# Performance work log

Measured on AMD Instinct MI355X. Metric: run time of the kernel, lower is better.

## Reference

```python
import jax, jax.numpy as jnp
import numpy as np

N = 500_000
D = 256
D_OUT = 256
B = 16_384


def setup_inputs() -> dict:
    key = jax.random.key(0)
    ks = jax.random.split(key, 10)
    x = jax.random.normal(ks[0], (N, D), dtype=jnp.float32)
    batch = jnp.sort(jax.random.randint(ks[1], (N,), 0, B))
    last_click_mask = jax.random.uniform(ks[2], (N,), dtype=jnp.float32)
    s = 1.0 / np.sqrt(D)
    W1 = jax.random.uniform(ks[3], (D, D), jnp.float32, -s, s)
    b1 = jax.random.uniform(ks[4], (D,), jnp.float32, -s, s)
    W2 = jax.random.uniform(ks[5], (D, D), jnp.float32, -s, s)
    b2 = jax.random.uniform(ks[6], (D,), jnp.float32, -s, s)
    w3 = jax.random.uniform(ks[7], (D, 1), jnp.float32, -s, s)
    s4 = 1.0 / np.sqrt(2 * D)
    W4 = jax.random.uniform(ks[8], (2 * D, D_OUT), jnp.float32, -s4, s4)
    b4 = jax.random.uniform(ks[9], (D_OUT,), jnp.float32, -s4, s4)
    return {
        "x": x,
        "batch": batch,
        "last_click_mask": last_click_mask,
        "num_segments": B,
        "W1": W1, "b1": b1, "W2": W2, "b2": b2,
        "w3": w3, "W4": W4, "b4": b4,
    }


def reference(x, batch, last_click_mask, num_segments, W1, b1, W2, b2, w3, W4, b4):
    # local_rep = global_add_pool(x * mask, batch)  -> [B, D]
    local_rep = jax.ops.segment_sum(x * last_click_mask[:, None], batch,
                                    num_segments=num_segments)
    local_rep_repeat = local_rep[batch]                       # [N, D] gather
    att = jax.nn.sigmoid(local_rep_repeat @ W1 + b1 + x @ W2 + b2) @ w3  # [N, 1]
    weighted_x = x * att                                      # [N, D]
    global_rep = jax.ops.segment_sum(weighted_x, batch,
                                     num_segments=num_segments)  # [B, D]
    rep = jnp.concatenate([local_rep, global_rep], axis=1)    # [B, 2D]
    return rep @ W4 + b4                                      # [B, D_OUT]
```

## Files before the change

### kernel.cpp

```cpp
#include <hip/hip_runtime.h>
#include <hip/hip_bf16.h>

#define NROWS 500000
#define DIM   256
#define BSEG  16384
#define LDSP  264

typedef __attribute__((ext_vector_type(8))) short short8;
typedef __attribute__((ext_vector_type(4))) float floatx4;


__device__ __forceinline__ unsigned short f2bf(float f) {
  unsigned u = __float_as_uint(f);
  unsigned r = u + 0x7fffu + ((u >> 16) & 1u);
  return (unsigned short)(r >> 16);
}
__device__ __forceinline__ float bf2f(short s) {
  return __uint_as_float(((unsigned)(unsigned short)s) << 16);
}
__device__ __forceinline__ float fast_sigmoid(float z) {
  return 1.0f / (1.0f + __expf(-z));
}

__global__ __launch_bounds__(1024) void k_zero(float* __restrict__ p, int n4) {
  int i = blockIdx.x * blockDim.x + threadIdx.x;
  if (i < n4) ((float4*)p)[i] = make_float4(0.f, 0.f, 0.f, 0.f);
}

__global__ __launch_bounds__(256) void k_convert_all(
    const float* __restrict__ W1, const float* __restrict__ W2,
    const float* __restrict__ W4, short* __restrict__ W1t,
    short* __restrict__ W2t, short* __restrict__ W4t)
{
  int blk = blockIdx.x;
  const float* W; short* out; int kt;
  if (blk < 8)       { W = W1; out = W1t; kt = blk; }
  else if (blk < 16) { W = W2; out = W2t; kt = blk - 8; }
  else               { W = W4; out = W4t; kt = blk - 16; }
  int n = threadIdx.x;
  short tmp[32];
#pragma unroll
  for (int kk = 0; kk < 32; ++kk)
    tmp[kk] = (short)f2bf(W[(size_t)(kt * 32 + kk) * DIM + n]);
  size_t base = ((size_t)kt * 256 + n) * 32;
#pragma unroll
  for (int kk = 0; kk < 32; kk += 4)
    *(short4*)&out[base + kk] = *(short4*)&tmp[kk];
}

__global__ __launch_bounds__(256) void k_seg_local(
    const float* __restrict__ x, const int* __restrict__ batch,
    const float* __restrict__ mask, float* __restrict__ local_rep,
    int rows_per_block)
{
  const int col = threadIdx.x;
  int r0 = blockIdx.x * rows_per_block;
  int r1 = min(NROWS, r0 + rows_per_block);
  if (r0 >= r1) return;
  float acc = 0.f;
  int cur = batch[r0];
  int r = r0;
  for (; r + 4 <= r1; r += 4) {
    float xv0 = x[(size_t)(r + 0) * DIM + col];
    float xv1 = x[(size_t)(r + 1) * DIM + col];
    float xv2 = x[(size_t)(r + 2) * DIM + col];
    float xv3 = x[(size_t)(r + 3) * DIM + col];
    int s0 = batch[r], s1 = batch[r + 1], s2 = batch[r + 2], s3 = batch[r + 3];
    float m0 = mask[r], m1 = mask[r + 1], m2 = mask[r + 2], m3 = mask[r + 3];
    if (s0 != cur) { atomicAdd(&local_rep[(size_t)cur * DIM + col], acc); acc = 0.f; cur = s0; }
    acc = fmaf(xv0, m0, acc);
    if (s1 != cur) { atomicAdd(&local_rep[(size_t)cur * DIM + col], acc); acc = 0.f; cur = s1; }
    acc = fmaf(xv1, m1, acc);
    if (s2 != cur) { atomicAdd(&local_rep[(size_t)cur * DIM + col], acc); acc = 0.f; cur = s2; }
    acc = fmaf(xv2, m2, acc);
    if (s3 != cur) { atomicAdd(&local_rep[(size_t)cur * DIM + col], acc); acc = 0.f; cur = s3; }
    acc = fmaf(xv3, m3, acc);
  }
  for (; r < r1; ++r) {
    int s = batch[r];
    float xv = x[(size_t)r * DIM + col];
    float mv = mask[r];
    if (s != cur) { atomicAdd(&local_rep[(size_t)cur * DIM + col], acc); acc = 0.f; cur = s; }
    acc = fmaf(xv, mv, acc);
  }
  atomicAdd(&local_rep[(size_t)cur * DIM + col], acc);
}

__device__ __forceinline__ void stage_tile(const float* __restrict__ A, int row0,
                                           int maxrow, short* xs, int tid)
{
#pragma unroll
  for (int it = 0; it < 16; ++it) {
    int linear = it * 256 + tid;
    int r = linear >> 6;
    int c4 = linear & 63;
    int row = min(row0 + r, maxrow);
    float4 v = *(const float4*)&A[(size_t)row * DIM + c4 * 4];
    short4 o;
    o.x = (short)f2bf(v.x); o.y = (short)f2bf(v.y);
    o.z = (short)f2bf(v.z); o.w = (short)f2bf(v.w);
    *(short4*)&xs[r * LDSP + c4 * 4] = o;
  }
}

__device__ __forceinline__ void mfma_pass(const short* xs, const short* __restrict__ Wt,
                                          floatx4 acc[4][4], int lane15, int quad, int n0)
{
  short8 bfr[2][4], afr[2][4];
#pragma unroll
  for (int jn = 0; jn < 4; ++jn)
    bfr[0][jn] = *(const short8*)&Wt[(size_t)(n0 + jn * 16 + lane15) * 32 + quad * 8];
#pragma unroll
  for (int i = 0; i < 4; ++i)
    afr[0][i] = *(const short8*)&xs[(i * 16 + lane15) * LDSP + quad * 8];

#pragma unroll
  for (int kt = 0; kt < 8; ++kt) {
    const int cur = kt & 1, nxt = cur ^ 1;
    if (kt < 7) {
      const int k2 = kt + 1;
#pragma unroll
      for (int jn = 0; jn < 4; ++jn)
        bfr[nxt][jn] = *(const short8*)&Wt[(size_t)k2 * 8192 + (n0 + jn * 16 + lane15) * 32 + quad * 8];
#pragma unroll
      for (int i = 0; i < 4; ++i)
        afr[nxt][i] = *(const short8*)&xs[(i * 16 + lane15) * LDSP + k2 * 32 + quad * 8];
    }
#pragma unroll
    for (int i = 0; i < 4; ++i)
#pragma unroll
      for (int jn = 0; jn < 4; ++jn)
        acc[i][jn] = __builtin_amdgcn_mfma_f32_16x16x32_bf16(afr[cur][i], bfr[cur][jn], acc[i][jn], 0, 0, 0);
  }
}

__global__ __launch_bounds__(256) void k_h1_mfma(
    const float* __restrict__ A, const short* __restrict__ Wt,
    const float* __restrict__ bias, short* __restrict__ H1bf)
{
  __shared__ short xs[64 * LDSP];
  const int tid = threadIdx.x;
  const int row0 = blockIdx.x * 64;
  stage_tile(A, row0, BSEG - 1, xs, tid);
  __syncthreads();
  const int lane = tid & 63, wave = tid >> 6;
  const int lane15 = lane & 15, quad = lane >> 4;
  const int n0 = wave * 64;
  floatx4 acc[4][4];
#pragma unroll
  for (int i = 0; i < 4; ++i)
#pragma unroll
    for (int j = 0; j < 4; ++j) acc[i][j] = (floatx4)0.f;
  mfma_pass(xs, Wt, acc, lane15, quad, n0);
#pragma unroll
  for (int i = 0; i < 4; ++i)
#pragma unroll
    for (int jn = 0; jn < 4; ++jn) {
      int col = n0 + jn * 16 + lane15;
      float bv = bias[col];
#pragma unroll
      for (int r = 0; r < 4; ++r) {
        int row = row0 + i * 16 + quad * 4 + r;
        H1bf[(size_t)row * DIM + col] = (short)f2bf(acc[i][jn][r] + bv);
      }
    }
}

__global__ __launch_bounds__(256) void k_fused_main(
    const float* __restrict__ x, const int* __restrict__ batch,
    const short* __restrict__ W2t, const float* __restrict__ b2,
    const float* __restrict__ w3, const short* __restrict__ H1bf,
    float* __restrict__ global_rep)
{
  __shared__ short xs[64 * LDSP];
  __shared__ int   seg_s[64];
  __shared__ float att_s[64];
  const int tid = threadIdx.x;
  const int row0 = blockIdx.x * 64;

  stage_tile(x, row0, NROWS - 1, xs, tid);
  if (tid < 64) {
    seg_s[tid] = batch[min(row0 + tid, NROWS - 1)];
    att_s[tid] = 0.f;
  }
  __syncthreads();

  const int lane = tid & 63, wave = tid >> 6;
  const int lane15 = lane & 15, quad = lane >> 4;
  const int n0 = wave * 64;
  floatx4 acc[4][4];
#pragma unroll
  for (int i = 0; i < 4; ++i)
#pragma unroll
    for (int j = 0; j < 4; ++j) acc[i][j] = (floatx4)0.f;
  mfma_pass(xs, W2t, acc, lane15, quad, n0);

  float b2v[4], w3v[4];
#pragma unroll
  for (int jn = 0; jn < 4; ++jn) {
    int col = n0 + jn * 16 + lane15;
    b2v[jn] = b2[col];
    w3v[jn] = w3[col];
  }
  float part[4][4];
#pragma unroll
  for (int i = 0; i < 4; ++i)
#pragma unroll
    for (int r = 0; r < 4; ++r) {
      int rl = i * 16 + quad * 4 + r;
      int seg = seg_s[rl];
      float p = 0.f;
#pragma unroll
      for (int jn = 0; jn < 4; ++jn) {
        int col = n0 + jn * 16 + lane15;
        float h = bf2f(H1bf[(size_t)seg * DIM + col]);
        float z = acc[i][jn][r] + h + b2v[jn];
        p = fmaf(fast_sigmoid(z), w3v[jn], p);
      }
      part[i][r] = p;
    }
#pragma unroll
  for (int off = 1; off < 16; off <<= 1)
#pragma unroll
    for (int i = 0; i < 4; ++i)
#pragma unroll
      for (int r = 0; r < 4; ++r)
        part[i][r] += __shfl_xor(part[i][r], off, 64);
  if (lane15 == 0) {
#pragma unroll
    for (int i = 0; i < 4; ++i)
#pragma unroll
      for (int r = 0; r < 4; ++r)
        atomicAdd(&att_s[i * 16 + quad * 4 + r], part[i][r]);
  }
  __syncthreads();

  const int col = tid;
  const int rmax = min(64, NROWS - row0);
  float acc2 = 0.f;
  int cur = seg_s[0];
  for (int r = 0; r < rmax; ++r) {
    int s = seg_s[r];
    float xv = bf2f(xs[r * LDSP + col]);
    float av = att_s[r];
    if (s != cur) {
      atomicAdd(&global_rep[(size_t)cur * DIM + col], acc2);
      acc2 = 0.f; cur = s;
    }
    acc2 = fmaf(xv, av, acc2);
  }
  atomicAdd(&global_rep[(size_t)cur * DIM + col], acc2);
}

__global__ __launch_bounds__(256) void k_out_mfma(
    const float* __restrict__ local_rep, const float* __restrict__ global_rep,
    const short* __restrict__ W4t, const float* __restrict__ b4,
    float* __restrict__ out)
{
  __shared__ short xs[64 * LDSP];
  const int tid = threadIdx.x;
  const int row0 = blockIdx.x * 64;
  const int lane = tid & 63, wave = tid >> 6;
  const int lane15 = lane & 15, quad = lane >> 4;
  const int n0 = wave * 64;
  floatx4 acc[4][4];
#pragma unroll
  for (int i = 0; i < 4; ++i)
#pragma unroll
    for (int j = 0; j < 4; ++j) acc[i][j] = (floatx4)0.f;

  stage_tile(local_rep, row0, BSEG - 1, xs, tid);
  __syncthreads();
  mfma_pass(xs, W4t, acc, lane15, quad, n0);
  __syncthreads();
  stage_tile(global_rep, row0, BSEG - 1, xs, tid);
  __syncthreads();
  mfma_pass(xs, W4t + (size_t)8 * 8192, acc, lane15, quad, n0);

#pragma unroll
  for (int i = 0; i < 4; ++i)
#pragma unroll
    for (int jn = 0; jn < 4; ++jn) {
      int col = n0 + jn * 16 + lane15;
      float bv = b4[col];
#pragma unroll
      for (int r = 0; r < 4; ++r) {
        int row = row0 + i * 16 + quad * 4 + r;
        out[(size_t)row * DIM + col] = acc[i][jn][r] + bv;
      }
    }
}

extern "C" void kernel_launch(void* const* d_in, const int* in_sizes, int n_in,
                              void* d_out, int out_size, void* d_ws, size_t ws_size,
                              hipStream_t stream) {
  (void)in_sizes; (void)n_in; (void)out_size; (void)ws_size;
  const float* x    = (const float*)d_in[0];
  const int*   batch= (const int*)d_in[1];
  const float* mask = (const float*)d_in[2];
  const float* W1 = (const float*)d_in[4];
  const float* b1 = (const float*)d_in[5];
  const float* W2 = (const float*)d_in[6];
  const float* b2 = (const float*)d_in[7];
  const float* w3 = (const float*)d_in[8];
  const float* W4 = (const float*)d_in[9];
  const float* b4 = (const float*)d_in[10];
  float* out = (float*)d_out;

  char* base = (char*)d_ws;
  float* local_rep  = (float*)(base);
  float* global_rep = (float*)(base + (size_t)16 * 1024 * 1024);
  short* H1bf       = (short*)(base + (size_t)32 * 1024 * 1024);
  short* W1t        = (short*)(base + (size_t)40 * 1024 * 1024);
  short* W2t        = (short*)(base + (size_t)40 * 1024 * 1024 + 128 * 1024);
  short* W4t        = (short*)(base + (size_t)40 * 1024 * 1024 + 256 * 1024);

  int n4 = 2 * BSEG * DIM / 4;
  hipLaunchKernelGGL(k_zero, dim3(n4 / 1024), dim3(1024), 0, stream, local_rep, n4);

  hipLaunchKernelGGL(k_convert_all, dim3(32), dim3(256), 0, stream,
                     W1, W2, W4, W1t, W2t, W4t);

  const int SEG_BLOCKS = 4096;
  int rpb = (NROWS + SEG_BLOCKS - 1) / SEG_BLOCKS;
  hipLaunchKernelGGL(k_seg_local, dim3(SEG_BLOCKS), dim3(256), 0, stream,
                     x, batch, mask, local_rep, rpb);

  hipLaunchKernelGGL(k_h1_mfma, dim3(BSEG / 64), dim3(256), 0, stream,
                     local_rep, W1t, b1, H1bf);

  hipLaunchKernelGGL(k_fused_main, dim3((NROWS + 63) / 64), dim3(256), 0, stream,
                     x, batch, W2t, b2, w3, H1bf, global_rep);

  hipLaunchKernelGGL(k_out_mfma, dim3(BSEG / 64), dim3(256), 0, stream,
                     local_rep, global_rep, W4t, b4, out);
}
```

Before: 1.023 ms.

## Pre-convert x to padded bf16 tiles and stream them into LDS directly

Replaces the strided segment-sum kernel with a tiled prep kernel. It stages each 64-row tile of x, converts it to bf16 and writes it out as a padded LDS image. It also computes the masked local segment sum from that tile. The main fused kernel then copies these bf16 tiles straight into LDS with global_load_lds instead of reloading fp32 x and converting it, which removes per-block conversion work and halves that kernel's input bytes. The MFMA inner loop also drops its register double-buffering, which reduces register pressure but may expose load latency. In exchange, the bf16 tile buffer is an extra write and read of roughly half the size of x, and local_rep is now summed from bf16-rounded x, which loses precision.

```diff
diff --git a/kernel.cpp b/kernel.cpp
--- a/kernel.cpp
+++ b/kernel.cpp
@@ -5,9 +5,16 @@
 #define DIM   256
 #define BSEG  16384
 #define LDSP  264
+#define NTILE 7813
+#define TILE_B (64 * LDSP * 2)
 
 typedef __attribute__((ext_vector_type(8))) short short8;
 typedef __attribute__((ext_vector_type(4))) float floatx4;
+
+#define GLD16(gsrc, ldst)                                                      \
+  __builtin_amdgcn_global_load_lds(                                            \
+      (const __attribute__((address_space(1))) unsigned int*)(gsrc),           \
+      (__attribute__((address_space(3))) unsigned int*)(ldst), 16, 0, 0)
 
 
 __device__ __forceinline__ unsigned short f2bf(float f) {
@@ -46,44 +53,6 @@
 #pragma unroll
   for (int kk = 0; kk < 32; kk += 4)
     *(short4*)&out[base + kk] = *(short4*)&tmp[kk];
-}
-
-__global__ __launch_bounds__(256) void k_seg_local(
-    const float* __restrict__ x, const int* __restrict__ batch,
-    const float* __restrict__ mask, float* __restrict__ local_rep,
-    int rows_per_block)
-{
-  const int col = threadIdx.x;
-  int r0 = blockIdx.x * rows_per_block;
-  int r1 = min(NROWS, r0 + rows_per_block);
-  if (r0 >= r1) return;
-  float acc = 0.f;
-  int cur = batch[r0];
-  int r = r0;
-  for (; r + 4 <= r1; r += 4) {
-    float xv0 = x[(size_t)(r + 0) * DIM + col];
-    float xv1 = x[(size_t)(r + 1) * DIM + col];
-    float xv2 = x[(size_t)(r + 2) * DIM + col];
-    float xv3 = x[(size_t)(r + 3) * DIM + col];
-    int s0 = batch[r], s1 = batch[r + 1], s2 = batch[r + 2], s3 = batch[r + 3];
-    float m0 = mask[r], m1 = mask[r + 1], m2 = mask[r + 2], m3 = mask[r + 3];
-    if (s0 != cur) { atomicAdd(&local_rep[(size_t)cur * DIM + col], acc); acc = 0.f; cur = s0; }
-    acc = fmaf(xv0, m0, acc);
-    if (s1 != cur) { atomicAdd(&local_rep[(size_t)cur * DIM + col], acc); acc = 0.f; cur = s1; }
-    acc = fmaf(xv1, m1, acc);
-    if (s2 != cur) { atomicAdd(&local_rep[(size_t)cur * DIM + col], acc); acc = 0.f; cur = s2; }
-    acc = fmaf(xv2, m2, acc);
-    if (s3 != cur) { atomicAdd(&local_rep[(size_t)cur * DIM + col], acc); acc = 0.f; cur = s3; }
-    acc = fmaf(xv3, m3, acc);
-  }
-  for (; r < r1; ++r) {
-    int s = batch[r];
-    float xv = x[(size_t)r * DIM + col];
-    float mv = mask[r];
-    if (s != cur) { atomicAdd(&local_rep[(size_t)cur * DIM + col], acc); acc = 0.f; cur = s; }
-    acc = fmaf(xv, mv, acc);
-  }
-  atomicAdd(&local_rep[(size_t)cur * DIM + col], acc);
 }
 
 __device__ __forceinline__ void stage_tile(const float* __restrict__ A, int row0,
@@ -103,34 +72,65 @@
   }
 }
 
+__global__ __launch_bounds__(256) void k_prep(
+    const float* __restrict__ x, const int* __restrict__ batch,
+    const float* __restrict__ mask, char* __restrict__ xbf16p,
+    float* __restrict__ local_rep)
+{
+  __shared__ __align__(16) short xs[64 * LDSP];
+  __shared__ int   seg_s[64];
+  __shared__ float mask_s[64];
+  const int tid = threadIdx.x;
+  const int tile = blockIdx.x;
+  const int row0 = tile * 64;
+
+  stage_tile(x, row0, NROWS - 1, xs, tid);
+  if (tid < 64) {
+    int row = min(row0 + tid, NROWS - 1);
+    seg_s[tid] = batch[row];
+    mask_s[tid] = mask[row];
+  }
+  __syncthreads();
+
+  float4* g4 = (float4*)(xbf16p + (size_t)tile * TILE_B);
+  const float4* l4 = (const float4*)xs;
+#pragma unroll
+  for (int j = 0; j < 8; ++j)
+    g4[j * 256 + tid] = l4[j * 256 + tid];
+  if (tid < 64) g4[2048 + tid] = l4[2048 + tid];
+
+  const int col = tid;
+  const int rmax = min(64, NROWS - row0);
+  float acc = 0.f;
+  int cur = seg_s[0];
+  for (int r = 0; r < rmax; ++r) {
+    int s = seg_s[r];
+    float xv = bf2f(xs[r * LDSP + col]);
+    if (s != cur) {
+      atomicAdd(&local_rep[(size_t)cur * DIM + col], acc);
+      acc = 0.f; cur = s;
+    }
+    acc = fmaf(xv, mask_s[r], acc);
+  }
+  atomicAdd(&local_rep[(size_t)cur * DIM + col], acc);
+}
+
 __device__ __forceinline__ void mfma_pass(const short* xs, const short* __restrict__ Wt,
                                           floatx4 acc[4][4], int lane15, int quad, int n0)
 {
-  short8 bfr[2][4], afr[2][4];
-#pragma unroll
-  for (int jn = 0; jn < 4; ++jn)
-    bfr[0][jn] = *(const short8*)&Wt[(size_t)(n0 + jn * 16 + lane15) * 32 + quad * 8];
-#pragma unroll
-  for (int i = 0; i < 4; ++i)
-    afr[0][i] = *(const short8*)&xs[(i * 16 + lane15) * LDSP + quad * 8];
-
-#pragma unroll
   for (int kt = 0; kt < 8; ++kt) {
-    const int cur = kt & 1, nxt = cur ^ 1;
-    if (kt < 7) {
-      const int k2 = kt + 1;
+    short8 bfr[4], afr[4];
+#pragma unroll
+    for (int jn = 0; jn < 4; ++jn)
+      bfr[jn] = *(const short8*)&Wt[(size_t)kt * 8192 + (n0 + jn * 16 + lane15) * 32 + quad * 8];
+#pragma unroll
+    for (int i = 0; i < 4; ++i)
+      afr[i] = *(const short8*)&xs[(i * 16 + lane15) * LDSP + kt * 32 + quad * 8];
+#pragma unroll
+    for (int i = 0; i < 4; ++i)
 #pragma unroll
       for (int jn = 0; jn < 4; ++jn)
-        bfr[nxt][jn] = *(const short8*)&Wt[(size_t)k2 * 8192 + (n0 + jn * 16 + lane15) * 32 + quad * 8];
-#pragma unroll
-      for (int i = 0; i < 4; ++i)
-        afr[nxt][i] = *(const short8*)&xs[(i * 16 + lane15) * LDSP + k2 * 32 + quad * 8];
-    }
-#pragma unroll
-    for (int i = 0; i < 4; ++i)
-#pragma unroll
-      for (int jn = 0; jn < 4; ++jn)
-        acc[i][jn] = __builtin_amdgcn_mfma_f32_16x16x32_bf16(afr[cur][i], bfr[cur][jn], acc[i][jn], 0, 0, 0);
+        acc[i][jn] = __builtin_amdgcn_mfma_f32_16x16x32_bf16(afr[i], bfr[jn], acc[i][jn], 0, 0, 0);
   }
 }
 
@@ -138,7 +138,7 @@
     const float* __restrict__ A, const short* __restrict__ Wt,
     const float* __restrict__ bias, short* __restrict__ H1bf)
 {
-  __shared__ short xs[64 * LDSP];
+  __shared__ __align__(16) short xs[64 * LDSP];
   const int tid = threadIdx.x;
   const int row0 = blockIdx.x * 64;
   stage_tile(A, row0, BSEG - 1, xs, tid);
@@ -167,25 +167,34 @@
 }
 
 __global__ __launch_bounds__(256) void k_fused_main(
-    const float* __restrict__ x, const int* __restrict__ batch,
+    const char* __restrict__ xbf16p, const int* __restrict__ batch,
     const short* __restrict__ W2t, const float* __restrict__ b2,
     const float* __restrict__ w3, const short* __restrict__ H1bf,
     float* __restrict__ global_rep)
 {
-  __shared__ short xs[64 * LDSP];
+  __shared__ __align__(16) short xs[64 * LDSP];
   __shared__ int   seg_s[64];
   __shared__ float att_s[64];
   const int tid = threadIdx.x;
   const int row0 = blockIdx.x * 64;
-
-  stage_tile(x, row0, NROWS - 1, xs, tid);
+  const int lane = tid & 63, wave = tid >> 6;
+
+  {
+    const char* gtile = xbf16p + (size_t)blockIdx.x * TILE_B;
+    char* lbase = (char*)xs;
+#pragma unroll
+    for (int j = 0; j < 9; ++j) {
+      int c = wave + 4 * j;
+      if (c < 33)
+        GLD16(gtile + (size_t)c * 1024 + lane * 16, lbase + c * 1024);
+    }
+  }
   if (tid < 64) {
     seg_s[tid] = batch[min(row0 + tid, NROWS - 1)];
     att_s[tid] = 0.f;
   }
   __syncthreads();
 
-  const int lane = tid & 63, wave = tid >> 6;
   const int lane15 = lane & 15, quad = lane >> 4;
   const int n0 = wave * 64;
   floatx4 acc[4][4];
@@ -257,7 +266,7 @@
     const short* __restrict__ W4t, const float* __restrict__ b4,
     float* __restrict__ out)
 {
-  __shared__ short xs[64 * LDSP];
+  __shared__ __align__(16) short xs[64 * LDSP];
   const int tid = threadIdx.x;
   const int row0 = blockIdx.x * 64;
   const int lane = tid & 63, wave = tid >> 6;
@@ -314,6 +323,7 @@
   short* W1t        = (short*)(base + (size_t)40 * 1024 * 1024);
   short* W2t        = (short*)(base + (size_t)40 * 1024 * 1024 + 128 * 1024);
   short* W4t        = (short*)(base + (size_t)40 * 1024 * 1024 + 256 * 1024);
+  char*  xbf16p     = base + (size_t)48 * 1024 * 1024;
 
   int n4 = 2 * BSEG * DIM / 4;
   hipLaunchKernelGGL(k_zero, dim3(n4 / 1024), dim3(1024), 0, stream, local_rep, n4);
@@ -321,16 +331,14 @@
   hipLaunchKernelGGL(k_convert_all, dim3(32), dim3(256), 0, stream,
                      W1, W2, W4, W1t, W2t, W4t);
 
-  const int SEG_BLOCKS = 4096;
-  int rpb = (NROWS + SEG_BLOCKS - 1) / SEG_BLOCKS;
-  hipLaunchKernelGGL(k_seg_local, dim3(SEG_BLOCKS), dim3(256), 0, stream,
-                     x, batch, mask, local_rep, rpb);
+  hipLaunchKernelGGL(k_prep, dim3(NTILE), dim3(256), 0, stream,
+                     x, batch, mask, xbf16p, local_rep);
 
   hipLaunchKernelGGL(k_h1_mfma, dim3(BSEG / 64), dim3(256), 0, stream,
                      local_rep, W1t, b1, H1bf);
 
-  hipLaunchKernelGGL(k_fused_main, dim3((NROWS + 63) / 64), dim3(256), 0, stream,
-                     x, batch, W2t, b2, w3, H1bf, global_rep);
+  hipLaunchKernelGGL(k_fused_main, dim3(NTILE), dim3(256), 0, stream,
+                     xbf16p, batch, W2t, b2, w3, H1bf, global_rep);
 
   hipLaunchKernelGGL(k_out_mfma, dim3(BSEG / 64), dim3(256), 0, stream,
                      local_rep, global_rep, W4t, b4, out);
```

Result: faster. 985.3 us (-3.7%).
